# Kernel optimization log

Hardware: AMD Instinct MI355X
Metric: run time of the kernel (lower is better)

Reference implementation:

```python
import jax, jax.numpy as jnp
import numpy as np

N = 100000
E = 1600000
D = 128
NUM_LAYERS = 3
NUM_QUANT = 3   # residual quantizer stages
K = 16          # codebook_size
COMMIT_W = 0.25


def setup_inputs() -> dict:
    key = jax.random.key(0)
    ks = jax.random.split(key, 6)
    x = jax.random.normal(ks[0], (N, D), dtype=jnp.float32)
    w_in = jax.random.normal(ks[1], (D, D), dtype=jnp.float32) / np.sqrt(D)
    b_in = jax.random.normal(ks[2], (D,), dtype=jnp.float32) * 0.01
    codebooks = jax.random.normal(ks[3], (NUM_LAYERS, NUM_QUANT, K, D), dtype=jnp.float32)
    edge_row = jax.random.randint(ks[4], (E,), 0, N, dtype=jnp.int32)
    edge_col = jax.random.randint(ks[5], (E,), 0, N, dtype=jnp.int32)
    return {"x": x, "w_in": w_in, "b_in": b_in, "codebooks": codebooks,
            "edge_row": edge_row, "edge_col": edge_col}


def _l2norm(v, eps=1e-12):
    return v / (jnp.linalg.norm(v, axis=-1, keepdims=True) + eps)


def _puregcn_conv(x, edge_row, edge_col):
    # norm = rsqrt(1 + deg); x = norm*x; x = spmm_add(adj, x) + x; x = norm*x
    n = x.shape[0]
    deg = jax.ops.segment_sum(jnp.ones_like(edge_row, dtype=x.dtype), edge_row, num_segments=n)
    norm = jax.lax.rsqrt(1.0 + deg)[:, None]
    h = norm * x
    agg = jax.ops.segment_sum(h[edge_col], edge_row, num_segments=n)  # [N, D]
    return norm * (agg + h)


def _residual_vq(x, cbs):
    # cbs: [NUM_QUANT, K, D]; cosine-sim lookup, EMA codebook (no grad to codebook)
    residual = x
    ids = []
    loss = jnp.float32(0.0)
    for q in range(NUM_QUANT):
        cb = _l2norm(cbs[q])                      # [K, D]
        sim = _l2norm(residual) @ cb.T            # [N, K]
        idx = jnp.argmax(sim, axis=-1)            # [N]
        qv = jax.lax.stop_gradient(cb[idx])       # [N, D]
        loss = loss + COMMIT_W * jnp.mean((residual - qv) ** 2)
        residual = residual - qv
        ids.append(idx.astype(jnp.int32))
    return jnp.stack(ids, axis=1), loss           # [N, NUM_QUANT], scalar


def reference(x, w_in, b_in, codebooks, edge_row, edge_col):
    # xemb: Linear (pure conv path); dropouts identity in eval
    h = x @ w_in + b_in
    id_list = []
    total_commit_loss = jnp.float32(0.0)
    for i in range(NUM_LAYERS):
        x1 = _puregcn_conv(h, edge_row, edge_col)   # lins[i] is Identity/Dropout(eval)
        ids, closs = _residual_vq(x1, codebooks[i])
        id_list.append(ids)
        total_commit_loss = total_commit_loss + closs
        h = x1 + h  # res=True, same width
    id_concat = jnp.concatenate(id_list, axis=1)    # [N, NUM_LAYERS*NUM_QUANT]
    return h, total_commit_loss, id_concat
```

## Files before the change

kernel.cpp:

```cpp
#include <hip/hip_runtime.h>

#define NN 100000
#define EE 1600000
#define DD 128
#define NL 3
#define NQ 3
#define KK 16
#define PADK 132
#define ROWS_PER_FBLOCK 32
#define FUSED_BLOCKS (NN / ROWS_PER_FBLOCK)
#define LPART_COUNT (NL * FUSED_BLOCKS)

static constexpr size_t OFF_AGG   = 0;
static constexpr size_t OFF_CSR   = 51200000;
static constexpr size_t OFF_CBN   = 57600000;
static constexpr size_t OFF_NORM  = 57904128;
static constexpr size_t OFF_DEG   = 58304128;
static constexpr size_t OFF_CUR   = 58704128;
static constexpr size_t OFF_RS    = 59104128;
static constexpr size_t OFF_BSUM  = 59504640;
static constexpr size_t OFF_LPART = 59505152;
static constexpr size_t WS_NEEDED = 59805152;

__global__ __launch_bounds__(256) void k_count(const int* __restrict__ erow,
                                               int* __restrict__ deg) {
    int e = blockIdx.x * 256 + threadIdx.x;
    if (e < EE) atomicAdd(&deg[erow[e]], 1);
}

__global__ __launch_bounds__(1024) void k_scan1(const int* __restrict__ deg,
                                                int* __restrict__ rs,
                                                int* __restrict__ bsum) {
    __shared__ int s[1024];
    int tid = threadIdx.x;
    int idx = blockIdx.x * 1024 + tid;
    int v = (idx < NN) ? deg[idx] : 0;
    s[tid] = v;
    __syncthreads();
    for (int o = 1; o < 1024; o <<= 1) {
        int t2 = s[tid];
        if (tid >= o) t2 += s[tid - o];
        __syncthreads();
        s[tid] = t2;
        __syncthreads();
    }
    if (idx < NN) rs[idx] = s[tid] - v;
    if (tid == 1023) bsum[blockIdx.x] = s[1023];
}

__global__ __launch_bounds__(128) void k_scan2(int* __restrict__ bsum, int nb) {
    __shared__ int s[128];
    int tid = threadIdx.x;
    int v = (tid < nb) ? bsum[tid] : 0;
    s[tid] = v;
    __syncthreads();
    for (int o = 1; o < 128; o <<= 1) {
        int t2 = s[tid];
        if (tid >= o) t2 += s[tid - o];
        __syncthreads();
        s[tid] = t2;
        __syncthreads();
    }
    if (tid < nb) bsum[tid] = s[tid] - v;
}

__global__ __launch_bounds__(1024) void k_scan3(const int* __restrict__ deg,
                                                int* __restrict__ rs,
                                                const int* __restrict__ bsum,
                                                float* __restrict__ normf) {
    int idx = blockIdx.x * 1024 + threadIdx.x;
    if (idx < NN) {
        rs[idx] += bsum[blockIdx.x];
        normf[idx] = rsqrtf(1.0f + (float)deg[idx]);
    }
    if (idx == 0) rs[NN] = EE;
}

__global__ __launch_bounds__(256) void k_fill(const int* __restrict__ erow,
                                              const int* __restrict__ ecol,
                                              const int* __restrict__ rs,
                                              int* __restrict__ cursor,
                                              int* __restrict__ csr) {
    int e = blockIdx.x * 256 + threadIdx.x;
    if (e < EE) {
        int r = erow[e];
        int p = atomicAdd(&cursor[r], 1);
        csr[rs[r] + p] = ecol[e];
    }
}

__global__ __launch_bounds__(256) void k_sortwave(const int* __restrict__ rs,
                                                  int* __restrict__ csr) {
    int wid = (blockIdx.x * 256 + threadIdx.x) >> 6;
    int l = threadIdx.x & 63;
    if (wid >= NN) return;
    int s0 = rs[wid], e0 = rs[wid + 1];
    int deg = e0 - s0;
    if (deg <= 1) return;
    if (deg <= 64) {
        int v = (l < deg) ? csr[s0 + l] : 0x7fffffff;
        int rank = 0;
#pragma unroll 8
        for (int m = 0; m < 64; ++m) {
            int vm = __shfl(v, m);
            bool less = (vm < v) || (vm == v && m < l);
            rank += (m < deg && less) ? 1 : 0;
        }
        if (l < deg) csr[s0 + rank] = v;
    } else if (l == 0) {
        for (int i = s0 + 1; i < e0; ++i) {
            int v = csr[i];
            int j = i - 1;
            while (j >= s0 && csr[j] > v) { csr[j + 1] = csr[j]; --j; }
            csr[j + 1] = v;
        }
    }
}

__global__ __launch_bounds__(128) void k_cbnorm(const float* __restrict__ cb,
                                                float* __restrict__ cbn) {
    __shared__ float s[128];
    int row = blockIdx.x;
    int tid = threadIdx.x;
    float v = cb[row * DD + tid];
    s[tid] = v * v;
    __syncthreads();
    for (int o = 64; o > 0; o >>= 1) {
        if (tid < o) s[tid] += s[tid + o];
        __syncthreads();
    }
    float inv = 1.0f / (sqrtf(s[0]) + 1e-12f);
    cbn[(size_t)row * PADK + tid] = v * inv;
}

__global__ __launch_bounds__(256) void k_gemm(const float* __restrict__ x,
                                              const float* __restrict__ w,
                                              const float* __restrict__ bias,
                                              float* __restrict__ h) {
    __shared__ float wls[64][DD];
    __shared__ float xs[32][DD];
    int tid = threadIdx.x;
    int rbase = blockIdx.x * 32;
    int cg = tid & 31;
    int rg = tid >> 5;

#pragma unroll
    for (int p = 0; p < 4; ++p) {
        int i = p * 256 + tid;
        int r = i >> 5, c = (i & 31) * 4;
        *(float4*)&xs[r][c] = *(const float4*)&x[(size_t)(rbase + r) * DD + c];
    }

    float4 acc[4];
#pragma unroll
    for (int i = 0; i < 4; ++i) acc[i] = make_float4(0.f, 0.f, 0.f, 0.f);

    for (int chunk = 0; chunk < 2; ++chunk) {
        __syncthreads();
#pragma unroll
        for (int p = 0; p < 8; ++p) {
            int i = p * 256 + tid;
            int kr = i >> 5, c = (i & 31) * 4;
            *(float4*)&wls[kr][c] = *(const float4*)&w[(size_t)(chunk * 64 + kr) * DD + c];
        }
        __syncthreads();
#pragma unroll 4
        for (int kk = 0; kk < 64; ++kk) {
            float4 wv = *(const float4*)&wls[kk][cg * 4];
            int k = chunk * 64 + kk;
#pragma unroll
            for (int i = 0; i < 4; ++i) {
                float xv = xs[rg * 4 + i][k];
                acc[i].x += xv * wv.x; acc[i].y += xv * wv.y;
                acc[i].z += xv * wv.z; acc[i].w += xv * wv.w;
            }
        }
    }

    float4 bv = *(const float4*)&bias[cg * 4];
#pragma unroll
    for (int i = 0; i < 4; ++i) {
        float4 o;
        o.x = acc[i].x + bv.x; o.y = acc[i].y + bv.y;
        o.z = acc[i].z + bv.z; o.w = acc[i].w + bv.w;
        *(float4*)&h[(size_t)(rbase + rg * 4 + i) * DD + cg * 4] = o;
    }
}

__global__ __launch_bounds__(256) void k_spmm(const float* __restrict__ h,
                                              const float* __restrict__ normf,
                                              const int* __restrict__ rs,
                                              const int* __restrict__ csr,
                                              float* __restrict__ agg) {
    int lane = threadIdx.x & 31;
    int slot = threadIdx.x >> 5;
    int r = blockIdx.x * 8 + slot;
    int s0 = rs[r], e0 = rs[r + 1];
    int off = lane << 2;

    float ax = 0.f, ay = 0.f, az = 0.f, aw = 0.f;
    int j = s0;
    for (; j + 4 <= e0; j += 4) {
        int c0 = csr[j], c1 = csr[j + 1], c2 = csr[j + 2], c3 = csr[j + 3];
        float n0 = normf[c0], n1 = normf[c1], n2 = normf[c2], n3 = normf[c3];
        float4 v0 = *(const float4*)&h[(size_t)c0 * DD + off];
        float4 v1 = *(const float4*)&h[(size_t)c1 * DD + off];
        float4 v2 = *(const float4*)&h[(size_t)c2 * DD + off];
        float4 v3 = *(const float4*)&h[(size_t)c3 * DD + off];
        ax += n0 * v0.x; ax += n1 * v1.x; ax += n2 * v2.x; ax += n3 * v3.x;
        ay += n0 * v0.y; ay += n1 * v1.y; ay += n2 * v2.y; ay += n3 * v3.y;
        az += n0 * v0.z; az += n1 * v1.z; az += n2 * v2.z; az += n3 * v3.z;
        aw += n0 * v0.w; aw += n1 * v1.w; aw += n2 * v2.w; aw += n3 * v3.w;
    }
    for (; j < e0; ++j) {
        int c = csr[j];
        float ns = normf[c];
        float4 v = *(const float4*)&h[(size_t)c * DD + off];
        ax += ns * v.x;
        ay += ns * v.y;
        az += ns * v.z;
        aw += ns * v.w;
    }
    float4 o = {ax, ay, az, aw};
    *(float4*)&agg[(size_t)r * DD + off] = o;
}

__global__ __launch_bounds__(256) void k_fused(const float* __restrict__ agg,
                                               float* __restrict__ h,
                                               const float* __restrict__ normf,
                                               const float* __restrict__ cbn_layer,
                                               float* __restrict__ idsf,
                                               float* __restrict__ lpart,
                                               int layer) {
    __shared__ float cb_s[NQ * KK * PADK];
    __shared__ float resid_s[4][DD];
    __shared__ float wsum[4];
    int tid = threadIdx.x;

    {
        const float4* src = (const float4*)cbn_layer;
        float4* dst = (float4*)cb_s;
        for (int i = tid; i < NQ * KK * PADK / 4; i += 256) dst[i] = src[i];
    }
    __syncthreads();

    int w = tid >> 6;
    int l = tid & 63;
    int kq = l >> 2;
    int sq = l & 3;
    float lsum = 0.f;

    for (int it = 0; it < ROWS_PER_FBLOCK / 4; ++it) {
        int r = blockIdx.x * ROWS_PER_FBLOCK + it * 4 + w;

        float nr = normf[r];
        float2 hv = *(const float2*)&h[(size_t)r * DD + 2 * l];
        float2 av = *(const float2*)&agg[(size_t)r * DD + 2 * l];
        float x0 = nr * (av.x + nr * hv.x);
        float x1 = nr * (av.y + nr * hv.y);
        float r0 = x0, r1 = x1;

        for (int q = 0; q < NQ; ++q) {
            *(float2*)&resid_s[w][2 * l] = make_float2(r0, r1);
            __syncthreads();

            const float* cbq = &cb_s[(q * KK + kq) * PADK];
            const float* rsd = resid_s[w];
            float pd = 0.f;
#pragma unroll
            for (int i = 0; i < 8; ++i) {
                float4 cv = *(const float4*)&cbq[sq * 32 + i * 4];
                float4 rv = *(const float4*)&rsd[sq * 32 + i * 4];
                pd += cv.x * rv.x + cv.y * rv.y + cv.z * rv.z + cv.w * rv.w;
            }
            pd += __shfl_xor(pd, 1);
            pd += __shfl_xor(pd, 2);

            float best = pd;
            int bk = kq;
            for (int m = 4; m < 64; m <<= 1) {
                float ov = __shfl_xor(best, m);
                int oi = __shfl_xor(bk, m);
                if (ov > best || (ov == best && oi < bk)) { best = ov; bk = oi; }
            }

            const float* cbk = &cb_s[(q * KK + bk) * PADK];
            float2 cv = *(const float2*)&cbk[2 * l];
            r0 -= cv.x;
            r1 -= cv.y;
            lsum += r0 * r0 + r1 * r1;

            if (l == 0) idsf[(size_t)r * (NL * NQ) + layer * NQ + q] = (float)bk;
            __syncthreads();
        }

        *(float2*)&h[(size_t)r * DD + 2 * l] = make_float2(x0 + hv.x, x1 + hv.y);
    }

#pragma unroll
    for (int m = 1; m < 64; m <<= 1) lsum += __shfl_xor(lsum, m);
    if (l == 0) wsum[w] = lsum;
    __syncthreads();
    if (tid == 0) {
        float tot = wsum[0] + wsum[1] + wsum[2] + wsum[3];
        lpart[layer * FUSED_BLOCKS + blockIdx.x] = tot * (0.25f / (float)(NN * DD));
    }
}

__global__ __launch_bounds__(256) void k_loss_reduce(const float* __restrict__ part,
                                                     float* __restrict__ out_loss) {
    __shared__ float s[256];
    float a = 0.f;
    for (int i = threadIdx.x; i < LPART_COUNT; i += 256) a += part[i];
    s[threadIdx.x] = a;
    __syncthreads();
    for (int o = 128; o > 0; o >>= 1) {
        if (threadIdx.x < o) s[threadIdx.x] += s[threadIdx.x + o];
        __syncthreads();
    }
    if (threadIdx.x == 0) out_loss[0] = s[0];
}

extern "C" void kernel_launch(void* const* d_in, const int* in_sizes, int n_in,
                              void* d_out, int out_size, void* d_ws, size_t ws_size,
                              hipStream_t stream) {
    if (ws_size < WS_NEEDED) return;

    const float* x    = (const float*)d_in[0];
    const float* w_in = (const float*)d_in[1];
    const float* b_in = (const float*)d_in[2];
    const float* cbs  = (const float*)d_in[3];
    const int*   erow = (const int*)d_in[4];
    const int*   ecol = (const int*)d_in[5];

    float* out  = (float*)d_out;
    float* hbuf = out;
    float* loss = out + (size_t)NN * DD;
    float* idsf = out + (size_t)NN * DD + 1;

    char* ws = (char*)d_ws;
    float* agg    = (float*)(ws + OFF_AGG);
    int*   csr    = (int*)(ws + OFF_CSR);
    float* cbn    = (float*)(ws + OFF_CBN);
    float* normf  = (float*)(ws + OFF_NORM);
    int*   deg    = (int*)(ws + OFF_DEG);
    int*   cursor = (int*)(ws + OFF_CUR);
    int*   rs     = (int*)(ws + OFF_RS);
    int*   bsum   = (int*)(ws + OFF_BSUM);
    float* lpart  = (float*)(ws + OFF_LPART);

    hipMemsetAsync(ws + OFF_DEG, 0, 800000, stream);

    const int NB_E  = (EE + 255) / 256;
    const int NB_SC = (NN + 1023) / 1024;
    const int NB_W  = (NN + 3) / 4;

    k_count<<<NB_E, 256, 0, stream>>>(erow, deg);
    k_scan1<<<NB_SC, 1024, 0, stream>>>(deg, rs, bsum);
    k_scan2<<<1, 128, 0, stream>>>(bsum, NB_SC);
    k_scan3<<<NB_SC, 1024, 0, stream>>>(deg, rs, bsum, normf);
    k_fill<<<NB_E, 256, 0, stream>>>(erow, ecol, rs, cursor, csr);
    k_sortwave<<<NB_W, 256, 0, stream>>>(rs, csr);

    k_cbnorm<<<NL * NQ * KK, 128, 0, stream>>>(cbs, cbn);
    k_gemm<<<NN / 32, 256, 0, stream>>>(x, w_in, b_in, hbuf);

    for (int layer = 0; layer < NL; ++layer) {
        k_spmm<<<NN / 8, 256, 0, stream>>>(hbuf, normf, rs, csr, agg);
        k_fused<<<FUSED_BLOCKS, 256, 0, stream>>>(agg, hbuf, normf,
                                                  cbn + (size_t)layer * NQ * KK * PADK,
                                                  idsf, lpart, layer);
    }

    k_loss_reduce<<<1, 256, 0, stream>>>(lpart, loss);
}
```

Measured before the change: 1.021 ms.

## Re-layout codebook and residual shared memory to avoid bank conflicts; unroll SpMM by 8

Rearranges the normalized codebook into an interleaved layout (stride 260 per 4-float chunk index, 16 floats per code) so that lanes computing dot products read consecutive float4s from LDS. It also pads the residual buffer (stride 36 per quarter-row) to avoid bank conflicts. Separately, the SpMM gather loop is unrolled by 8 to keep more independent loads in flight. The cost is more complex indexing and higher register pressure in SpMM.

```diff
diff --git a/kernel.cpp b/kernel.cpp
--- a/kernel.cpp
+++ b/kernel.cpp
@@ -6,10 +6,15 @@
 #define NL 3
 #define NQ 3
 #define KK 16
-#define PADK 132
 #define ROWS_PER_FBLOCK 32
 #define FUSED_BLOCKS (NN / ROWS_PER_FBLOCK)
 #define LPART_COUNT (NL * FUSED_BLOCKS)
+
+#define ISTRIDE 260
+#define QSTRIDE (8 * ISTRIDE)
+#define LAYER_CBN (NQ * QSTRIDE)
+#define RSTRIDE 36
+#define RBUF 144
 
 static constexpr size_t OFF_AGG   = 0;
 static constexpr size_t OFF_CSR   = 51200000;
@@ -130,7 +135,10 @@
         __syncthreads();
     }
     float inv = 1.0f / (sqrtf(s[0]) + 1e-12f);
-    cbn[(size_t)row * PADK + tid] = v * inv;
+    int lq = row >> 4;
+    int k  = row & 15;
+    int sq = tid >> 5, ii = (tid >> 2) & 7, d = tid & 3;
+    cbn[(size_t)lq * QSTRIDE + ii * ISTRIDE + k * 16 + sq * 4 + d] = v * inv;
 }
 
 __global__ __launch_bounds__(256) void k_gemm(const float* __restrict__ x,
@@ -200,6 +208,28 @@
 
     float ax = 0.f, ay = 0.f, az = 0.f, aw = 0.f;
     int j = s0;
+    for (; j + 8 <= e0; j += 8) {
+        int c0 = csr[j],     c1 = csr[j + 1], c2 = csr[j + 2], c3 = csr[j + 3];
+        int c4 = csr[j + 4], c5 = csr[j + 5], c6 = csr[j + 6], c7 = csr[j + 7];
+        float n0 = normf[c0], n1 = normf[c1], n2 = normf[c2], n3 = normf[c3];
+        float n4 = normf[c4], n5 = normf[c5], n6 = normf[c6], n7 = normf[c7];
+        float4 v0 = *(const float4*)&h[(size_t)c0 * DD + off];
+        float4 v1 = *(const float4*)&h[(size_t)c1 * DD + off];
+        float4 v2 = *(const float4*)&h[(size_t)c2 * DD + off];
+        float4 v3 = *(const float4*)&h[(size_t)c3 * DD + off];
+        float4 v4 = *(const float4*)&h[(size_t)c4 * DD + off];
+        float4 v5 = *(const float4*)&h[(size_t)c5 * DD + off];
+        float4 v6 = *(const float4*)&h[(size_t)c6 * DD + off];
+        float4 v7 = *(const float4*)&h[(size_t)c7 * DD + off];
+        ax += n0 * v0.x; ax += n1 * v1.x; ax += n2 * v2.x; ax += n3 * v3.x;
+        ax += n4 * v4.x; ax += n5 * v5.x; ax += n6 * v6.x; ax += n7 * v7.x;
+        ay += n0 * v0.y; ay += n1 * v1.y; ay += n2 * v2.y; ay += n3 * v3.y;
+        ay += n4 * v4.y; ay += n5 * v5.y; ay += n6 * v6.y; ay += n7 * v7.y;
+        az += n0 * v0.z; az += n1 * v1.z; az += n2 * v2.z; az += n3 * v3.z;
+        az += n4 * v4.z; az += n5 * v5.z; az += n6 * v6.z; az += n7 * v7.z;
+        aw += n0 * v0.w; aw += n1 * v1.w; aw += n2 * v2.w; aw += n3 * v3.w;
+        aw += n4 * v4.w; aw += n5 * v5.w; aw += n6 * v6.w; aw += n7 * v7.w;
+    }
     for (; j + 4 <= e0; j += 4) {
         int c0 = csr[j], c1 = csr[j + 1], c2 = csr[j + 2], c3 = csr[j + 3];
         float n0 = normf[c0], n1 = normf[c1], n2 = normf[c2], n3 = normf[c3];
@@ -232,22 +262,23 @@
                                                float* __restrict__ idsf,
                                                float* __restrict__ lpart,
                                                int layer) {
-    __shared__ float cb_s[NQ * KK * PADK];
-    __shared__ float resid_s[4][DD];
+    __shared__ float cb_s[LAYER_CBN];
+    __shared__ float resid_s[4][RBUF];
     __shared__ float wsum[4];
     int tid = threadIdx.x;
 
     {
         const float4* src = (const float4*)cbn_layer;
         float4* dst = (float4*)cb_s;
-        for (int i = tid; i < NQ * KK * PADK / 4; i += 256) dst[i] = src[i];
+        for (int t = tid; t < LAYER_CBN / 4; t += 256) dst[t] = src[t];
     }
     __syncthreads();
 
     int w = tid >> 6;
     int l = tid & 63;
-    int kq = l >> 2;
+    int rwrd = (l >> 4) * RSTRIDE + ((2 * l) & 31);
     int sq = l & 3;
+    int cb2 = ((l >> 1) & 7) * ISTRIDE + (l >> 4) * 4 + 2 * (l & 1);
     float lsum = 0.f;
 
     for (int it = 0; it < ROWS_PER_FBLOCK / 4; ++it) {
@@ -261,33 +292,32 @@
         float r0 = x0, r1 = x1;
 
         for (int q = 0; q < NQ; ++q) {
-            *(float2*)&resid_s[w][2 * l] = make_float2(r0, r1);
+            *(float2*)&resid_s[w][rwrd] = make_float2(r0, r1);
             __syncthreads();
 
-            const float* cbq = &cb_s[(q * KK + kq) * PADK];
+            const float* cbq = &cb_s[q * QSTRIDE];
             const float* rsd = resid_s[w];
             float pd = 0.f;
 #pragma unroll
             for (int i = 0; i < 8; ++i) {
-                float4 cv = *(const float4*)&cbq[sq * 32 + i * 4];
-                float4 rv = *(const float4*)&rsd[sq * 32 + i * 4];
+                float4 cv = *(const float4*)&cbq[i * ISTRIDE + l * 4];
+                float4 rv = *(const float4*)&rsd[sq * RSTRIDE + i * 4];
                 pd += cv.x * rv.x + cv.y * rv.y + cv.z * rv.z + cv.w * rv.w;
             }
             pd += __shfl_xor(pd, 1);
             pd += __shfl_xor(pd, 2);
 
             float best = pd;
-            int bk = kq;
+            int bk = l >> 2;
             for (int m = 4; m < 64; m <<= 1) {
                 float ov = __shfl_xor(best, m);
                 int oi = __shfl_xor(bk, m);
                 if (ov > best || (ov == best && oi < bk)) { best = ov; bk = oi; }
             }
 
-            const float* cbk = &cb_s[(q * KK + bk) * PADK];
-            float2 cv = *(const float2*)&cbk[2 * l];
-            r0 -= cv.x;
-            r1 -= cv.y;
+            float2 cv2 = *(const float2*)&cb_s[q * QSTRIDE + bk * 16 + cb2];
+            r0 -= cv2.x;
+            r1 -= cv2.y;
             lsum += r0 * r0 + r1 * r1;
 
             if (l == 0) idsf[(size_t)r * (NL * NQ) + layer * NQ + q] = (float)bk;
@@ -368,7 +398,7 @@
     for (int layer = 0; layer < NL; ++layer) {
         k_spmm<<<NN / 8, 256, 0, stream>>>(hbuf, normf, rs, csr, agg);
         k_fused<<<FUSED_BLOCKS, 256, 0, stream>>>(agg, hbuf, normf,
-                                                  cbn + (size_t)layer * NQ * KK * PADK,
+                                                  cbn + (size_t)layer * LAYER_CBN,
                                                   idsf, lpart, layer);
     }
 
```

Measured after the change: 913.1 us. -10.5%, faster.
